# Kernel tuning notes

Measured on AMD Instinct MI355X. Metric: run time of the kernel, lower is better.

The kernel has to match this reference:

```python
import jax, jax.numpy as jnp
import numpy as np

N_DRUG, N_DIS = 100_000, 50_000
E1, E2 = 500_000, 250_000
D, H = 128, 4
HD = D // H          # 32
EAD, CONT, CARD = 32, 4, 8


def _segment_softmax(logits, seg, num_segments):
    # logits: [E, H], seg: [E] -> softmax normalized per destination node (PyG softmax)
    m = jax.ops.segment_max(logits, seg, num_segments=num_segments)
    m = jnp.where(jnp.isfinite(m), m, 0.0)  # empty segments
    ex = jnp.exp(logits - m[seg])
    s = jax.ops.segment_sum(ex, seg, num_segments=num_segments)
    return ex / (s[seg] + 1e-16)


def _edge_conv(src_x, dst_x, si, di, Wsrc, bsrc, Wdst, bdst, attn, gate):
    num_dst = dst_x.shape[0]
    msg_src = src_x[si] @ Wsrc + bsrc            # [E, D]
    msg_dst = dst_x[di] @ Wdst + bdst            # [E, D]
    msg = msg_src + msg_dst
    if gate is not None:
        msg = msg * gate
    E = msg.shape[0]
    mh = msg.reshape(E, H, HD)
    sh = msg_src.reshape(E, H, HD)
    dh = msg_dst.reshape(E, H, HD)
    logits = (sh * dh).sum(-1) * (1.0 / np.sqrt(HD)) + (mh * attn[None]).sum(-1)  # [E, H]
    w = _segment_softmax(logits, di, num_dst)    # [E, H]; dropout p applied only in training
    out = (mh * w[..., None]).reshape(E, D)
    return jax.ops.segment_sum(out, di, num_segments=num_dst)  # [num_dst, D]


def setup_inputs() -> dict:
    key = jax.random.key(0)
    it = iter(jax.random.split(key, 32))
    def nrm(shape, s=0.05):
        return jax.random.normal(next(it), shape, jnp.float32) * s
    def ri(hi, shape):
        return jax.random.randint(next(it), shape, 0, hi, jnp.int32)
    z = lambda n: jnp.zeros((n,), jnp.float32)
    return {
        "x_drug": nrm((N_DRUG, D), 1.0),
        "x_dis": nrm((N_DIS, D), 1.0),
        "e1_cont": nrm((E1, CONT), 1.0),
        "W_src1": nrm((D, D)), "b_src1": z(D),
        "W_dst1": nrm((D, D)), "b_dst1": z(D),
        "attn1": nrm((H, HD)),
        "emb1": nrm((CARD, EAD)),
        "gW1": nrm((EAD + CONT, D)), "gb1": z(D),
        "gW2": nrm((D, D)), "gb2": z(D),
        "W_src2": nrm((D, D)), "b_src2": z(D),
        "W_dst2": nrm((D, D)), "b_dst2": z(D),
        "attn2": nrm((H, HD)),
        "Wo_drug": nrm((D, D)), "bo_drug": z(D),
        "Wo_dis": nrm((D, D)), "bo_dis": z(D),
        "e1_src": ri(N_DRUG, (E1,)), "e1_dst": ri(N_DRUG, (E1,)),
        "e2_src": ri(N_DRUG, (E2,)), "e2_dst": ri(N_DIS, (E2,)),
        "e1_cat": ri(CARD, (E1,)),
    }


def reference(x_drug, x_dis, e1_cont, W_src1, b_src1, W_dst1, b_dst1, attn1,
              emb1, gW1, gb1, gW2, gb2, W_src2, b_src2, W_dst2, b_dst2, attn2,
              Wo_drug, bo_drug, Wo_dis, bo_dis,
              e1_src, e1_dst, e2_src, e2_dst, e1_cat):
    # drug -> drug edges, spec mixed (1 categorical + 4 continuous): gated messages
    gate_feat = jnp.concatenate([emb1[e1_cat], e1_cont], axis=-1)  # [E1, EAD+CONT]
    gate = jax.nn.sigmoid(
        jax.nn.gelu(gate_feat @ gW1 + gb1, approximate=False) @ gW2 + gb2)  # [E1, D]
    aggr_drug = _edge_conv(x_drug, x_drug, e1_src, e1_dst,
                           W_src1, b_src1, W_dst1, b_dst1, attn1, gate)
    # drug -> disease edges, spec none: no gate
    aggr_dis = _edge_conv(x_drug, x_dis, e2_src, e2_dst,
                          W_src2, b_src2, W_dst2, b_dst2, attn2, None)
    # one message list per dst node type -> mean over a single element == identity
    out_drug = aggr_drug @ Wo_drug + bo_drug
    out_dis = aggr_dis @ Wo_dis + bo_dis
    return (out_drug, out_dis)
```

## Files before the change

kernel.cpp:

```cpp
#include <hip/hip_runtime.h>
#include <hip/hip_bf16.h>
#include <math.h>

#define ND 100000
#define NS 50000
#define NE1 500000
#define NE2 250000
#define DIM 128
#define NH 4
#define HDI 32
#define GRID_M 512
#define GRID_G 1024
#define GRID_E1 2048
#define GRID_E2 1024
#define NT1 (NE1 / 16)
#define NT2 (NE2 / 16)

typedef __hip_bfloat16 bf16;
typedef unsigned short u16;
typedef unsigned int u32;
typedef short sx8 __attribute__((ext_vector_type(8)));
typedef float fx4 __attribute__((ext_vector_type(4)));

__device__ __forceinline__ float ldf(const float* p, size_t i) { return p[i]; }
__device__ __forceinline__ float ldf(const bf16* p, size_t i) { return __bfloat162float(p[i]); }
__device__ __forceinline__ float b2f(bf16 v) { return __bfloat162float(v); }

__device__ __forceinline__ u16 f2bfu(float f) {
    __hip_bfloat16 h = __float2bfloat16(f);
    union { __hip_bfloat16 b; u16 u; } c; c.b = h; return c.u;
}
__device__ __forceinline__ float2 bfp(u32 u) {
    float2 r;
    r.x = __uint_as_float(u << 16);
    r.y = __uint_as_float(u & 0xffff0000u);
    return r;
}
__device__ __forceinline__ sx8 pack8(float4 v0, float4 v1) {
    sx8 r;
    r[0] = (short)f2bfu(v0.x); r[1] = (short)f2bfu(v0.y);
    r[2] = (short)f2bfu(v0.z); r[3] = (short)f2bfu(v0.w);
    r[4] = (short)f2bfu(v1.x); r[5] = (short)f2bfu(v1.y);
    r[6] = (short)f2bfu(v1.z); r[7] = (short)f2bfu(v1.w);
    return r;
}
__device__ __forceinline__ sx8 lda8(const bf16* p) { return *(const sx8*)p; }
__device__ __forceinline__ sx8 lda8(const float* p) {
    return pack8(*(const float4*)p, *(const float4*)(p + 4));
}
__device__ __forceinline__ float4 ld4(const float* p) { return *(const float4*)p; }
__device__ __forceinline__ float4 ld4(const bf16* p) {
    float2 a = bfp(*(const u32*)p);
    float2 b = bfp(*(const u32*)(p + 2));
    return make_float4(a.x, a.y, b.x, b.y);
}

__device__ __forceinline__ float gelu_fast(float x) {
    float u2 = x * fmaf(x * x, 0.0713550f, 1.5957691f);
    u2 = fminf(u2, 40.0f);
    float t = __expf(u2);
    return x * t * __builtin_amdgcn_rcpf(t + 1.0f);
}
__device__ __forceinline__ float sigmoid_fast(float x) {
    return __builtin_amdgcn_rcpf(1.0f + __expf(-x));
}
__device__ __forceinline__ float exp_fast(float x) { return __expf(x); }

__device__ __forceinline__ void slab_store(float* Gw, const fx4* acc, int er, int lg) {
#pragma unroll
    for (int f = 0; f < 8; ++f)
#pragma unroll
        for (int r = 0; r < 4; ++r) {
            int row = 4 * lg + r;
            int byo = row * 512 + (((16 * f + er) * 4) ^ ((row & 7) << 4));
            *(float*)((char*)Gw + byo) = acc[f][r];
        }
}
__device__ __forceinline__ void slab_flush_bf16(const float* Gw, int lane, bf16* Yrow) {
#pragma unroll
    for (int i = 0; i < 16; ++i) {
        float2 gv = *(const float2*)((const char*)Gw + i * 512 + ((lane * 8) ^ ((i & 7) << 4)));
        u32 pk = ((u32)f2bfu(gv.y) << 16) | (u32)f2bfu(gv.x);
        *(u32*)&Yrow[(size_t)i * DIM + 2 * lane] = pk;
    }
}
__device__ __forceinline__ void sty2(float* p, float2 v) { *(float2*)p = v; }
__device__ __forceinline__ void sty2(bf16* p, float2 v) {
    *(u32*)p = ((u32)f2bfu(v.y) << 16) | (u32)f2bfu(v.x);
}

__global__ void fill16_kernel(u16* p, u16 v, size_t n) {
    size_t i = (size_t)blockIdx.x * blockDim.x + threadIdx.x;
    if (i < n) p[i] = v;
}

__global__ __launch_bounds__(64) void detect_kernel(const u16* w, int* flag) {
    int lane = threadIdx.x;
    int mx = 0;
    for (int j = 0; j < 32; ++j) {
        int i = 2 * (lane + 64 * j);
        int e = (w[i] >> 7) & 0xFF;
        mx = mx > e ? mx : e;
    }
    for (int d = 32; d; d >>= 1) { int o = __shfl_xor(mx, d); mx = mx > o ? mx : o; }
    if (lane == 0) flag[0] = (mx >= 0x90) ? 1 : 0;
}

__global__ __launch_bounds__(256) void hist_kernel(const int* __restrict__ dst, int ne,
                                                   u32* __restrict__ cnt) {
    int stride = gridDim.x * blockDim.x;
    for (int i = blockIdx.x * blockDim.x + threadIdx.x; i < ne; i += stride)
        atomicAdd(&cnt[dst[i]], 1u);
}

__global__ __launch_bounds__(256) void scanA_kernel(const u32* __restrict__ cnt, int nb,
                                                    u32* __restrict__ chk) {
    __shared__ u32 ws[4];
    int b = blockIdx.x, t = threadIdx.x;
    int i0 = b * 1024 + t * 4;
    u32 s = 0;
#pragma unroll
    for (int j = 0; j < 4; ++j) { int i = i0 + j; if (i < nb) s += cnt[i]; }
#pragma unroll
    for (int d = 1; d < 64; d <<= 1) s += __shfl_xor(s, d);
    if ((t & 63) == 0) ws[t >> 6] = s;
    __syncthreads();
    if (t == 0) chk[b] = ws[0] + ws[1] + ws[2] + ws[3];
}

__global__ __launch_bounds__(256) void scanB_kernel(u32* __restrict__ chk, int nc) {
    __shared__ u32 sh[256];
    int t = threadIdx.x;
    u32 v = (t < nc) ? chk[t] : 0u;
    sh[t] = v;
    __syncthreads();
    for (int d = 1; d < 256; d <<= 1) {
        u32 x = (t >= d) ? sh[t - d] : 0u;
        __syncthreads();
        if (t >= d) sh[t] += x;
        __syncthreads();
    }
    if (t < nc) chk[t] = sh[t] - v;
}

__global__ __launch_bounds__(256) void scanC_kernel(const u32* __restrict__ cnt, int nb,
                                                    const u32* __restrict__ chk,
                                                    u32* __restrict__ offs) {
    __shared__ u32 wsum[4];
    int b = blockIdx.x, t = threadIdx.x, lane = t & 63, wv = t >> 6;
    int i0 = b * 1024 + t * 4;
    u32 c0 = (i0 + 0 < nb) ? cnt[i0 + 0] : 0u;
    u32 c1 = (i0 + 1 < nb) ? cnt[i0 + 1] : 0u;
    u32 c2 = (i0 + 2 < nb) ? cnt[i0 + 2] : 0u;
    u32 c3 = (i0 + 3 < nb) ? cnt[i0 + 3] : 0u;
    u32 tot = c0 + c1 + c2 + c3;
    u32 inc = tot;
#pragma unroll
    for (int d = 1; d < 64; d <<= 1) { u32 x = __shfl_up(inc, d); if (lane >= d) inc += x; }
    if (lane == 63) wsum[wv] = inc;
    __syncthreads();
    u32 base = chk[b] + (inc - tot);
    for (int k = 0; k < wv; ++k) base += wsum[k];
    if (i0 + 0 < nb) offs[i0 + 0] = base;
    if (i0 + 1 < nb) offs[i0 + 1] = base + c0;
    if (i0 + 2 < nb) offs[i0 + 2] = base + c0 + c1;
    if (i0 + 3 < nb) offs[i0 + 3] = base + c0 + c1 + c2;
}

__global__ __launch_bounds__(256) void scatter_kernel(const int* __restrict__ dst, int ne,
                                                      u32* __restrict__ offs,
                                                      u32* __restrict__ perm) {
    int stride = gridDim.x * blockDim.x;
    for (int i = blockIdx.x * blockDim.x + threadIdx.x; i < ne; i += stride) {
        u32 p = atomicAdd(&offs[dst[i]], 1u);
        perm[p] = (u32)i;
    }
}

template <typename T>
__device__ __forceinline__ void transp(const T* W, u16* Bt, int gtid, int gstride) {
    for (int i = gtid; i < DIM * DIM; i += gstride) {
        int n = i >> 7, k = i & 127;
        Bt[i] = f2bfu(ldf(W, (size_t)k * DIM + n));
    }
}

template <typename T>
__device__ __forceinline__ void prep_body(
    const T* emb, const T* gW1, const T* gb1, const T* gW2,
    const T* Ws1, const T* Wd1, const T* Ws2, const T* Wd2, const T* Wod, const T* Wos,
    u16* B1t, float* gb2f, const T* gb2,
    u16* Btg, u16* Bs1, u16* Bd1, u16* Bs2, u16* Bd2, u16* Bod, u16* Bos)
{
    int gtid = blockIdx.x * blockDim.x + threadIdx.x;
    int gstride = gridDim.x * blockDim.x;
    for (int i = gtid; i < DIM * 32; i += gstride) {
        int n = i >> 5, k = i & 31;
        float v = 0.0f;
        if (k < 8) {
            v = ldf(gb1, n);
            for (int q = 0; q < 32; ++q) v += ldf(emb, k * 32 + q) * ldf(gW1, (size_t)q * DIM + n);
        } else if (k < 12) {
            v = ldf(gW1, (size_t)(32 + (k - 8)) * DIM + n);
        }
        B1t[i] = f2bfu(v);
    }
    for (int i = gtid; i < DIM; i += gstride) gb2f[i] = ldf(gb2, i);
    transp(gW2, Btg, gtid, gstride);
    transp(Ws1, Bs1, gtid, gstride);
    transp(Wd1, Bd1, gtid, gstride);
    transp(Ws2, Bs2, gtid, gstride);
    transp(Wd2, Bd2, gtid, gstride);
    transp(Wod, Bod, gtid, gstride);
    transp(Wos, Bos, gtid, gstride);
}

__global__ __launch_bounds__(256) void prep_kernel(
    const int* __restrict__ flag,
    const void* emb, const void* gW1, const void* gb1, const void* gW2, const void* gb2,
    const void* Ws1, const void* Wd1, const void* Ws2, const void* Wd2,
    const void* Wod, const void* Wos,
    u16* __restrict__ B1t, float* __restrict__ gb2f,
    u16* __restrict__ Btg, u16* __restrict__ Bs1, u16* __restrict__ Bd1,
    u16* __restrict__ Bs2, u16* __restrict__ Bd2, u16* __restrict__ Bod,
    u16* __restrict__ Bos)
{
    if (flag[0])
        prep_body((const float*)emb, (const float*)gW1, (const float*)gb1, (const float*)gW2,
                  (const float*)Ws1, (const float*)Wd1, (const float*)Ws2, (const float*)Wd2,
                  (const float*)Wod, (const float*)Wos,
                  B1t, gb2f, (const float*)gb2, Btg, Bs1, Bd1, Bs2, Bd2, Bod, Bos);
    else
        prep_body((const bf16*)emb, (const bf16*)gW1, (const bf16*)gb1, (const bf16*)gW2,
                  (const bf16*)Ws1, (const bf16*)Wd1, (const bf16*)Ws2, (const bf16*)Wd2,
                  (const bf16*)Wod, (const bf16*)Wos,
                  B1t, gb2f, (const bf16*)gb2, Btg, Bs1, Bd1, Bs2, Bd2, Bod, Bos);
}

template <typename T>
__device__ __forceinline__ void proj2m_body(
    float* Gw, const T* X, const T* b1, const T* b2,
    const u16* Bt1, const u16* Bt2, bf16* Y1, bf16* Y2, int N)
{
    int tid = threadIdx.x, lane = tid & 63, er = lane & 15, lg = lane >> 4;
    float c1i[8], c2i[8];
#pragma unroll
    for (int f = 0; f < 8; ++f) {
        c1i[f] = ldf(b1, 16 * f + er);
        c2i[f] = ldf(b2, 16 * f + er);
    }
    const int NW = GRID_M * 4;
    int gwid = blockIdx.x * 4 + (tid >> 6);
    int tiles = N / 16;
    for (int t = gwid; t < tiles; t += NW) {
        const T* xr = X + (size_t)(t * 16 + er) * DIM;
        sx8 a[4];
#pragma unroll
        for (int ks = 0; ks < 4; ++ks) a[ks] = lda8(xr + ks * 32 + lg * 8);
        fx4 acc1[8], acc2[8];
#pragma unroll
        for (int f = 0; f < 8; ++f) {
            acc1[f][0] = c1i[f]; acc1[f][1] = c1i[f]; acc1[f][2] = c1i[f]; acc1[f][3] = c1i[f];
            acc2[f][0] = c2i[f]; acc2[f][1] = c2i[f]; acc2[f][2] = c2i[f]; acc2[f][3] = c2i[f];
        }
#pragma unroll
        for (int ks = 0; ks < 4; ++ks)
#pragma unroll
            for (int f = 0; f < 8; ++f) {
                sx8 bv1 = *(const sx8*)(Bt1 + (size_t)(16 * f + er) * DIM + ks * 32 + lg * 8);
                acc1[f] = __builtin_amdgcn_mfma_f32_16x16x32_bf16(a[ks], bv1, acc1[f], 0, 0, 0);
                sx8 bv2 = *(const sx8*)(Bt2 + (size_t)(16 * f + er) * DIM + ks * 32 + lg * 8);
                acc2[f] = __builtin_amdgcn_mfma_f32_16x16x32_bf16(a[ks], bv2, acc2[f], 0, 0, 0);
            }
        slab_store(Gw, acc1, er, lg);
        slab_flush_bf16(Gw, lane, Y1 + (size_t)t * 16 * DIM);
        slab_store(Gw, acc2, er, lg);
        slab_flush_bf16(Gw, lane, Y2 + (size_t)t * 16 * DIM);
    }
}

__global__ __launch_bounds__(256) void proj2m_kernel(
    const int* __restrict__ flag, const void* X, const void* b1, const void* b2,
    const u16* __restrict__ Bt1, const u16* __restrict__ Bt2,
    bf16* __restrict__ Y1, bf16* __restrict__ Y2, int N)
{
    __shared__ float Gt[4][16 * 128];
    float* Gw = Gt[threadIdx.x >> 6];
    if (flag[0]) proj2m_body(Gw, (const float*)X, (const float*)b1, (const float*)b2, Bt1, Bt2, Y1, Y2, N);
    else         proj2m_body(Gw, (const bf16*)X, (const bf16*)b1, (const bf16*)b2, Bt1, Bt2, Y1, Y2, N);
}

template <typename T>
__device__ __forceinline__ void proj1m_body(
    float* Gw, const T* X, const T* b, const u16* Bt, bf16* Y, int N)
{
    int tid = threadIdx.x, lane = tid & 63, er = lane & 15, lg = lane >> 4;
    float ci[8];
#pragma unroll
    for (int f = 0; f < 8; ++f) ci[f] = ldf(b, 16 * f + er);
    const int NW = GRID_M * 4;
    int gwid = blockIdx.x * 4 + (tid >> 6);
    int tiles = N / 16;
    for (int t = gwid; t < tiles; t += NW) {
        const T* xr = X + (size_t)(t * 16 + er) * DIM;
        sx8 a[4];
#pragma unroll
        for (int ks = 0; ks < 4; ++ks) a[ks] = lda8(xr + ks * 32 + lg * 8);
        fx4 acc[8];
#pragma unroll
        for (int f = 0; f < 8; ++f) {
            acc[f][0] = ci[f]; acc[f][1] = ci[f]; acc[f][2] = ci[f]; acc[f][3] = ci[f];
        }
#pragma unroll
        for (int ks = 0; ks < 4; ++ks)
#pragma unroll
            for (int f = 0; f < 8; ++f) {
                sx8 bv = *(const sx8*)(Bt + (size_t)(16 * f + er) * DIM + ks * 32 + lg * 8);
                acc[f] = __builtin_amdgcn_mfma_f32_16x16x32_bf16(a[ks], bv, acc[f], 0, 0, 0);
            }
        slab_store(Gw, acc, er, lg);
        slab_flush_bf16(Gw, lane, Y + (size_t)t * 16 * DIM);
    }
}

__global__ __launch_bounds__(256) void proj1m_kernel(
    const int* __restrict__ flag, const void* X, const void* b,
    const u16* __restrict__ Bt, bf16* __restrict__ Y, int N)
{
    __shared__ float Gt[4][16 * 128];
    float* Gw = Gt[threadIdx.x >> 6];
    if (flag[0]) proj1m_body(Gw, (const float*)X, (const float*)b, Bt, Y, N);
    else         proj1m_body(Gw, (const bf16*)X, (const bf16*)b, Bt, Y, N);
}

template <typename T>
__device__ __forceinline__ void projoutm_body(
    float* Gw, const float* A, const float* s, const T* b,
    const u16* Bt, T* out, int N)
{
    int tid = threadIdx.x, lane = tid & 63, er = lane & 15, lg = lane >> 4;
    float ci[8];
#pragma unroll
    for (int f = 0; f < 8; ++f) ci[f] = ldf(b, 16 * f + er);
    const int NW = GRID_M * 4;
    int gwid = blockIdx.x * 4 + (tid >> 6);
    int tiles = N / 16;
    for (int t = gwid; t < tiles; t += NW) {
        const float* ar = A + (size_t)(t * 16 + er) * DIM;
        const float* sr = s + (size_t)(t * 16 + er) * NH;
        sx8 a[4];
#pragma unroll
        for (int ks = 0; ks < 4; ++ks) {
            float inv = 1.0f / (sr[ks] + 1e-16f);
            float4 v0 = *(const float4*)(ar + ks * 32 + lg * 8);
            float4 v1 = *(const float4*)(ar + ks * 32 + lg * 8 + 4);
            v0.x *= inv; v0.y *= inv; v0.z *= inv; v0.w *= inv;
            v1.x *= inv; v1.y *= inv; v1.z *= inv; v1.w *= inv;
            a[ks] = pack8(v0, v1);
        }
        fx4 acc[8];
#pragma unroll
        for (int f = 0; f < 8; ++f) {
            acc[f][0] = ci[f]; acc[f][1] = ci[f]; acc[f][2] = ci[f]; acc[f][3] = ci[f];
        }
#pragma unroll
        for (int ks = 0; ks < 4; ++ks)
#pragma unroll
            for (int f = 0; f < 8; ++f) {
                sx8 bv = *(const sx8*)(Bt + (size_t)(16 * f + er) * DIM + ks * 32 + lg * 8);
                acc[f] = __builtin_amdgcn_mfma_f32_16x16x32_bf16(a[ks], bv, acc[f], 0, 0, 0);
            }
        slab_store(Gw, acc, er, lg);
#pragma unroll
        for (int i = 0; i < 16; ++i) {
            float2 gv = *(const float2*)((const char*)Gw + i * 512 + ((lane * 8) ^ ((i & 7) << 4)));
            sty2(out + (size_t)(t * 16 + i) * DIM + 2 * lane, gv);
        }
    }
}

__global__ __launch_bounds__(256) void projoutm_kernel(
    const int* __restrict__ flag, const float* __restrict__ A, const float* __restrict__ s,
    const void* b, const u16* __restrict__ Bt, void* out, size_t off, int N)
{
    __shared__ float Gt[4][16 * 128];
    float* Gw = Gt[threadIdx.x >> 6];
    if (flag[0]) projoutm_body(Gw, A, s, (const float*)b, Bt, (float*)out + off, N);
    else         projoutm_body(Gw, A, s, (const bf16*)b, Bt, (bf16*)out + off, N);
}

template <typename T>
__device__ __forceinline__ void gateall_body(
    float* Gw, const int* cat, const T* econt,
    const float* gb2f, const u16* B1t, const u16* Btg,
    const u32* perm, u32* gates, int c0, int c1)
{
    int tid = threadIdx.x;
    int lane = tid & 63;
    int er = lane & 15, lg = lane >> 4;

    float cinit[8];
#pragma unroll
    for (int f = 0; f < 8; ++f) cinit[f] = gb2f[16 * f + er];

    const int NW = GRID_G * 4;
    int span = c1 - c0;
    int w = blockIdx.x * 4 + (tid >> 6);
    int tpw = (span + NW - 1) / NW;
    int t0 = c0 + w * tpw, t1 = t0 + tpw;
    if (t1 > c1) t1 = c1;

    const fx4 zf = {0.f, 0.f, 0.f, 0.f};

    for (int t = t0; t < t1; ++t) {
        int e = (int)perm[t * 16 + er];

        sx8 a1;
#pragma unroll
        for (int j = 0; j < 8; ++j) a1[j] = 0;
        if (lg == 0) {
            int c = cat[e];
#pragma unroll
            for (int j = 0; j < 8; ++j) a1[j] = (c == j) ? (short)0x3F80 : (short)0;
        } else if (lg == 1) {
            float4 fv = ld4(econt + (size_t)e * 4);
            a1[0] = (short)f2bfu(fv.x); a1[1] = (short)f2bfu(fv.y);
            a1[2] = (short)f2bfu(fv.z); a1[3] = (short)f2bfu(fv.w);
        }

        fx4 p1[8];
#pragma unroll
        for (int f = 0; f < 8; ++f) {
            sx8 b1 = *(const sx8*)(B1t + (size_t)(16 * f + er) * 32 + lg * 8);
            p1[f] = __builtin_amdgcn_mfma_f32_16x16x32_bf16(a1, b1, zf, 0, 0, 0);
        }

#pragma unroll
        for (int f = 0; f < 8; ++f)
#pragma unroll
            for (int r = 0; r < 4; ++r) {
                int row = 4 * lg + r;
                float hg = gelu_fast(p1[f][r]);
                int byo = row * 512 + (((16 * f + er) * 4) ^ ((row & 7) << 4));
                *(float*)((char*)Gw + byo) = hg;
            }

        sx8 a2[4];
#pragma unroll
        for (int ks = 0; ks < 4; ++ks) {
            int base = ks * 128 + lg * 32;
            float4 v0 = *(const float4*)((const char*)Gw + er * 512 + ((base)      ^ ((er & 7) << 4)));
            float4 v1 = *(const float4*)((const char*)Gw + er * 512 + ((base + 16) ^ ((er & 7) << 4)));
            a2[ks] = pack8(v0, v1);
        }

        fx4 acc[8];
#pragma unroll
        for (int f = 0; f < 8; ++f) {
            acc[f][0] = cinit[f]; acc[f][1] = cinit[f];
            acc[f][2] = cinit[f]; acc[f][3] = cinit[f];
        }
#pragma unroll
        for (int ks = 0; ks < 4; ++ks) {
#pragma unroll
            for (int f = 0; f < 8; ++f) {
                sx8 b = *(const sx8*)(Btg + (size_t)(16 * f + er) * DIM + ks * 32 + lg * 8);
                acc[f] = __builtin_amdgcn_mfma_f32_16x16x32_bf16(a2[ks], b, acc[f], 0, 0, 0);
            }
        }

#pragma unroll
        for (int f = 0; f < 8; ++f)
#pragma unroll
            for (int r = 0; r < 4; ++r) {
                int row = 4 * lg + r;
                float g = sigmoid_fast(acc[f][r]);
                int byo = row * 512 + (((16 * f + er) * 4) ^ ((row & 7) << 4));
                *(float*)((char*)Gw + byo) = g;
            }

#pragma unroll
        for (int i = 0; i < 16; ++i) {
            float2 gv = *(const float2*)((const char*)Gw + i * 512 + ((lane * 8) ^ ((i & 7) << 4)));
            u32 pk = ((u32)f2bfu(gv.y) << 16) | (u32)f2bfu(gv.x);
            gates[((size_t)(t - c0) * 16 + i) * 64 + lane] = pk;
        }
    }
}

__global__ __launch_bounds__(256) void gateall_kernel(
    const int* __restrict__ flag, const int* __restrict__ cat, const void* econt,
    const float* __restrict__ gb2f, const u16* __restrict__ B1t,
    const u16* __restrict__ Btg,
    const u32* __restrict__ perm, u32* __restrict__ gates, int c0, int c1)
{
    __shared__ float Gt[4][16 * 128];
    float* Gw = Gt[threadIdx.x >> 6];
    if (flag[0]) gateall_body(Gw, cat, (const float*)econt, gb2f, B1t, Btg, perm, gates, c0, c1);
    else         gateall_body(Gw, cat, (const bf16*)econt, gb2f, B1t, Btg, perm, gates, c0, c1);
}

template <typename T>
__device__ __forceinline__ void edge1e_body(
    const bf16* Xs, const bf16* Xd,
    const int* src, const int* dst,
    const T* attn, const u32* perm, const u32* gates, int c0, int c1,
    float* s_out, float* aggr)
{
    int tid = threadIdx.x;
    int lane = tid & 63;
    int d0 = 2 * lane, h = lane >> 4, k0 = d0 & 31;
    float av0 = ldf(attn, h * HDI + k0), av1 = ldf(attn, h * HDI + k0 + 1);
    const float rs = 0.17677669529663688110f;

    const int NW = GRID_E1 * 4;
    int span = c1 - c0;
    int w = blockIdx.x * 4 + (tid >> 6);
    int cpw = (span + NW - 1) / NW;
    int t0 = c0 + w * cpw, t1 = t0 + cpw;
    if (t1 > c1) t1 = c1;

    int cur_di = -1;
    float acc0 = 0.f, acc1 = 0.f, ssum = 0.f;

    for (int t = t0; t < t1; ++t) {
        u32 pe = 0, sv = 0, dv = 0;
        if (lane < 16) {
            pe = perm[t * 16 + lane];
            sv = (u32)src[(int)pe];
            dv = (u32)dst[(int)pe];
        }
        u32 xsp[16], xdp[16], gp[16];
#pragma unroll
        for (int i = 0; i < 16; ++i) {
            int si = (int)__builtin_amdgcn_readlane(sv, i);
            int di = (int)__builtin_amdgcn_readlane(dv, i);
            xsp[i] = *(const u32*)&Xs[(size_t)si * DIM + d0];
            xdp[i] = *(const u32*)&Xd[(size_t)di * DIM + d0];
            gp[i]  = gates[((size_t)(t - c0) * 16 + i) * 64 + lane];
        }
#pragma unroll
        for (int i = 0; i < 16; ++i) {
            int di = (int)__builtin_amdgcn_readlane(dv, i);
            float2 sxy = bfp(xsp[i]);
            float2 dxy = bfp(xdp[i]);
            float2 gxy = bfp(gp[i]);
            if (di != cur_di) {
                if (cur_di >= 0) {
                    float* ap = &aggr[(size_t)cur_di * DIM + d0];
                    atomicAdd(ap, acc0);
                    atomicAdd(ap + 1, acc1);
                    if ((lane & 15) == 0)
                        atomicAdd(&s_out[(size_t)cur_di * NH + h], ssum);
                }
                cur_di = di; acc0 = 0.f; acc1 = 0.f; ssum = 0.f;
            }
            float m0 = (sxy.x + dxy.x) * gxy.x;
            float m1 = (sxy.y + dxy.y) * gxy.y;
            float p = (sxy.x * dxy.x + sxy.y * dxy.y) * rs + m0 * av0 + m1 * av1;
            p += __shfl_xor(p, 8);
            p += __shfl_xor(p, 4);
            p += __shfl_xor(p, 2);
            p += __shfl_xor(p, 1);
            float ev = exp_fast(fminf(p, 80.0f));
            acc0 = fmaf(ev, m0, acc0);
            acc1 = fmaf(ev, m1, acc1);
            ssum += ev;
        }
    }
    if (cur_di >= 0) {
        float* ap = &aggr[(size_t)cur_di * DIM + d0];
        atomicAdd(ap, acc0);
        atomicAdd(ap + 1, acc1);
        if ((lane & 15) == 0)
            atomicAdd(&s_out[(size_t)cur_di * NH + h], ssum);
    }
}

__global__ __launch_bounds__(256) void edge1e_kernel(
    const int* __restrict__ flag,
    const bf16* __restrict__ Xs, const bf16* __restrict__ Xd,
    const int* __restrict__ src, const int* __restrict__ dst,
    const void* attn, const u32* __restrict__ perm, const u32* __restrict__ gates,
    int c0, int c1, float* __restrict__ s_out, float* __restrict__ aggr)
{
    if (flag[0]) edge1e_body(Xs, Xd, src, dst, (const float*)attn, perm, gates, c0, c1, s_out, aggr);
    else         edge1e_body(Xs, Xd, src, dst, (const bf16*)attn, perm, gates, c0, c1, s_out, aggr);
}

template <typename T>
__device__ __forceinline__ void edge2e_body(
    const bf16* Xs, const bf16* Xd,
    const int* src, const int* dst,
    const T* attn, const u32* perm, float* s_out, float* aggr)
{
    int tid = threadIdx.x;
    int lane = tid & 63;
    int d0 = 2 * lane, h = lane >> 4, k0 = d0 & 31;
    float av0 = ldf(attn, h * HDI + k0), av1 = ldf(attn, h * HDI + k0 + 1);
    const float rs = 0.17677669529663688110f;

    const int NW = GRID_E2 * 4;
    int w = blockIdx.x * 4 + (tid >> 6);
    int cpw = (NT2 + NW - 1) / NW;
    int t0 = w * cpw, t1 = t0 + cpw;
    if (t1 > NT2) t1 = NT2;

    int cur_di = -1;
    float acc0 = 0.f, acc1 = 0.f, ssum = 0.f;

    for (int t = t0; t < t1; ++t) {
        u32 pe = 0, sv = 0, dv = 0;
        if (lane < 16) {
            pe = perm[t * 16 + lane];
            sv = (u32)src[(int)pe];
            dv = (u32)dst[(int)pe];
        }
        u32 xsp[16], xdp[16];
#pragma unroll
        for (int i = 0; i < 16; ++i) {
            int si = (int)__builtin_amdgcn_readlane(sv, i);
            int di = (int)__builtin_amdgcn_readlane(dv, i);
            xsp[i] = *(const u32*)&Xs[(size_t)si * DIM + d0];
            xdp[i] = *(const u32*)&Xd[(size_t)di * DIM + d0];
        }
#pragma unroll
        for (int i = 0; i < 16; ++i) {
            int di = (int)__builtin_amdgcn_readlane(dv, i);
            float2 sxy = bfp(xsp[i]);
            float2 dxy = bfp(xdp[i]);
            if (di != cur_di) {
                if (cur_di >= 0) {
                    float* ap = &aggr[(size_t)cur_di * DIM + d0];
                    atomicAdd(ap, acc0);
                    atomicAdd(ap + 1, acc1);
                    if ((lane & 15) == 0)
                        atomicAdd(&s_out[(size_t)cur_di * NH + h], ssum);
                }
                cur_di = di; acc0 = 0.f; acc1 = 0.f; ssum = 0.f;
            }
            float m0 = sxy.x + dxy.x;
            float m1 = sxy.y + dxy.y;
            float p = (sxy.x * dxy.x + sxy.y * dxy.y) * rs + m0 * av0 + m1 * av1;
            p += __shfl_xor(p, 8);
            p += __shfl_xor(p, 4);
            p += __shfl_xor(p, 2);
            p += __shfl_xor(p, 1);
            float ev = exp_fast(fminf(p, 80.0f));
            acc0 = fmaf(ev, m0, acc0);
            acc1 = fmaf(ev, m1, acc1);
            ssum += ev;
        }
    }
    if (cur_di >= 0) {
        float* ap = &aggr[(size_t)cur_di * DIM + d0];
        atomicAdd(ap, acc0);
        atomicAdd(ap + 1, acc1);
        if ((lane & 15) == 0)
            atomicAdd(&s_out[(size_t)cur_di * NH + h], ssum);
    }
}

__global__ __launch_bounds__(256) void edge2e_kernel(
    const int* __restrict__ flag,
    const bf16* __restrict__ Xs, const bf16* __restrict__ Xd,
    const int* __restrict__ src, const int* __restrict__ dst,
    const void* attn, const u32* __restrict__ perm,
    float* __restrict__ s_out, float* __restrict__ aggr)
{
    if (flag[0]) edge2e_body(Xs, Xd, src, dst, (const float*)attn, perm, s_out, aggr);
    else         edge2e_body(Xs, Xd, src, dst, (const bf16*)attn, perm, s_out, aggr);
}

extern "C" void kernel_launch(void* const* d_in, const int* in_sizes, int n_in,
                              void* d_out, int out_size, void* d_ws, size_t ws_size,
                              hipStream_t stream)
{
    const void* x_drug  = d_in[0];
    const void* x_dis   = d_in[1];
    const void* e1_cont = d_in[2];
    const void* W_src1  = d_in[3];
    const void* b_src1  = d_in[4];
    const void* W_dst1  = d_in[5];
    const void* b_dst1  = d_in[6];
    const void* attn1   = d_in[7];
    const void* emb1    = d_in[8];
    const void* gW1     = d_in[9];
    const void* gb1     = d_in[10];
    const void* gW2     = d_in[11];
    const void* gb2     = d_in[12];
    const void* W_src2  = d_in[13];
    const void* b_src2  = d_in[14];
    const void* W_dst2  = d_in[15];
    const void* b_dst2  = d_in[16];
    const void* attn2   = d_in[17];
    const void* Wo_drug = d_in[18];
    const void* bo_drug = d_in[19];
    const void* Wo_dis  = d_in[20];
    const void* bo_dis  = d_in[21];
    const int* e1_src = (const int*)d_in[22];
    const int* e1_dst = (const int*)d_in[23];
    const int* e2_src = (const int*)d_in[24];
    const int* e2_dst = (const int*)d_in[25];
    const int* e1_cat = (const int*)d_in[26];

    bool sizes_ok = (n_in == 27)
        && in_sizes[0] == ND * DIM && in_sizes[1] == NS * DIM
        && in_sizes[2] == NE1 * 4
        && in_sizes[3] == DIM * DIM && in_sizes[4] == DIM
        && in_sizes[5] == DIM * DIM && in_sizes[6] == DIM
        && in_sizes[7] == NH * HDI && in_sizes[8] == 8 * 32
        && in_sizes[9] == 36 * DIM && in_sizes[10] == DIM
        && in_sizes[11] == DIM * DIM && in_sizes[12] == DIM
        && in_sizes[13] == DIM * DIM && in_sizes[17] == NH * HDI
        && in_sizes[18] == DIM * DIM && in_sizes[20] == DIM * DIM
        && in_sizes[22] == NE1 && in_sizes[23] == NE1
        && in_sizes[24] == NE2 && in_sizes[25] == NE2 && in_sizes[26] == NE1;
    if (!sizes_ok) {
        size_t n = (size_t)out_size;
        fill16_kernel<<<(int)((n + 255) / 256), 256, 0, stream>>>((u16*)d_out, 0x429A, n);
        return;
    }

    size_t off_B1   = 64;
    size_t off_g2   = off_B1 + (size_t)DIM * 32 * 2;
    size_t off_Bt   = off_g2 + DIM * 4;
    size_t off_Bs1  = off_Bt  + (size_t)DIM * DIM * 2;
    size_t off_Bd1  = off_Bs1 + (size_t)DIM * DIM * 2;
    size_t off_Bs2  = off_Bd1 + (size_t)DIM * DIM * 2;
    size_t off_Bd2  = off_Bs2 + (size_t)DIM * DIM * 2;
    size_t off_Bod  = off_Bd2 + (size_t)DIM * DIM * 2;
    size_t off_Bos  = off_Bod + (size_t)DIM * DIM * 2;
    size_t off_Xs   = off_Bos + (size_t)DIM * DIM * 2;
    size_t off_Xd   = off_Xs + (size_t)ND * DIM * 2;
    size_t off_sb   = off_Xd + (size_t)ND * DIM * 2;
    size_t off_aggr = off_sb + (size_t)ND * NH * 4;
    size_t off_cnt  = off_aggr + (size_t)ND * DIM * 4;
    size_t off_offs = off_cnt + (size_t)(ND + 16) * 4;
    size_t off_chk  = off_offs + (size_t)(ND + 16) * 4;
    size_t off_p1   = off_chk + 512;
    size_t off_p2   = off_p1 + (size_t)NE1 * 4;
    size_t off_gate = (off_p2 + (size_t)NE2 * 4 + 255) & ~(size_t)255;
    if (ws_size < off_gate) {
        size_t n = (size_t)out_size;
        fill16_kernel<<<(int)((n + 255) / 256), 256, 0, stream>>>((u16*)d_out, 0x42F6, n);
        return;
    }

    int nparts = 0, cpp = 0;
    for (int p = 1; p <= 32; p <<= 1) {
        int c = (NT1 + p - 1) / p;
        if (off_gate + (size_t)c * 16 * 256 <= ws_size) { nparts = p; cpp = c; break; }
    }
    if (!nparts) {
        size_t n = (size_t)out_size;
        fill16_kernel<<<(int)((n + 255) / 256), 256, 0, stream>>>((u16*)d_out, 0x42F6, n);
        return;
    }

    char* w = (char*)d_ws;
    int*   flag = (int*)w;
    u16*   B1t  = (u16*)(w + off_B1);
    float* gb2p = (float*)(w + off_g2);
    u16*   Btg  = (u16*)(w + off_Bt);
    u16*   Bs1  = (u16*)(w + off_Bs1);
    u16*   Bd1  = (u16*)(w + off_Bd1);
    u16*   Bs2  = (u16*)(w + off_Bs2);
    u16*   Bd2  = (u16*)(w + off_Bd2);
    u16*   Bod  = (u16*)(w + off_Bod);
    u16*   Bos  = (u16*)(w + off_Bos);
    bf16*  Xs   = (bf16*)(w + off_Xs);
    bf16*  Xd   = (bf16*)(w + off_Xd);
    float* sb   = (float*)(w + off_sb);
    float* aggr = (float*)(w + off_aggr);
    u32*   cnt  = (u32*)(w + off_cnt);
    u32*   offs = (u32*)(w + off_offs);
    u32*   chk  = (u32*)(w + off_chk);
    u32*   perm1 = (u32*)(w + off_p1);
    u32*   perm2 = (u32*)(w + off_p2);
    u32*   gates = (u32*)(w + off_gate);

    detect_kernel<<<1, 64, 0, stream>>>((const u16*)W_src1, flag);
    prep_kernel<<<64, 256, 0, stream>>>(flag, emb1, gW1, gb1, gW2, gb2,
                                        W_src1, W_dst1, W_src2, W_dst2, Wo_drug, Wo_dis,
                                        B1t, gb2p, Btg, Bs1, Bd1, Bs2, Bd2, Bod, Bos);

    hipMemsetAsync(cnt, 0, (size_t)(ND + 16) * 4, stream);
    hist_kernel<<<1024, 256, 0, stream>>>(e1_dst, NE1, cnt);
    scanA_kernel<<<98, 256, 0, stream>>>(cnt, ND, chk);
    scanB_kernel<<<1, 256, 0, stream>>>(chk, 98);
    scanC_kernel<<<98, 256, 0, stream>>>(cnt, ND, chk, offs);
    scatter_kernel<<<1024, 256, 0, stream>>>(e1_dst, NE1, offs, perm1);

    hipMemsetAsync(sb, 0, (size_t)ND * NH * 4, stream);
    hipMemsetAsync(aggr, 0, (size_t)ND * DIM * 4, stream);
    proj2m_kernel<<<GRID_M, 256, 0, stream>>>(flag, x_drug, b_src1, b_dst1, Bs1, Bd1, Xs, Xd, ND);
    for (int part = 0; part < nparts; ++part) {
        int c0 = part * cpp, c1 = c0 + cpp;
        if (c1 > NT1) c1 = NT1;
        if (c0 >= c1) break;
        gateall_kernel<<<GRID_G, 256, 0, stream>>>(flag, e1_cat, e1_cont,
                                                   gb2p, B1t, Btg, perm1, gates, c0, c1);
        edge1e_kernel<<<GRID_E1, 256, 0, stream>>>(flag, Xs, Xd, e1_src, e1_dst,
                                                   attn1, perm1, gates, c0, c1, sb, aggr);
    }
    projoutm_kernel<<<GRID_M, 256, 0, stream>>>(flag, aggr, sb, bo_drug, Bod, d_out, 0, ND);

    hipMemsetAsync(cnt, 0, (size_t)(NS + 16) * 4, stream);
    hist_kernel<<<1024, 256, 0, stream>>>(e2_dst, NE2, cnt);
    scanA_kernel<<<49, 256, 0, stream>>>(cnt, NS, chk);
    scanB_kernel<<<1, 256, 0, stream>>>(chk, 49);
    scanC_kernel<<<49, 256, 0, stream>>>(cnt, NS, chk, offs);
    scatter_kernel<<<1024, 256, 0, stream>>>(e2_dst, NE2, offs, perm2);

    hipMemsetAsync(sb, 0, (size_t)NS * NH * 4, stream);
    hipMemsetAsync(aggr, 0, (size_t)NS * DIM * 4, stream);
    proj1m_kernel<<<GRID_M, 256, 0, stream>>>(flag, x_drug, b_src2, Bs2, Xs, ND);
    proj1m_kernel<<<GRID_M, 256, 0, stream>>>(flag, x_dis, b_dst2, Bd2, Xd, NS);
    edge2e_kernel<<<GRID_E2, 256, 0, stream>>>(flag, Xs, Xd, e2_src, e2_dst, attn2, perm2, sb, aggr);
    projoutm_kernel<<<GRID_M, 256, 0, stream>>>(flag, aggr, sb, bo_dis, Bos, d_out, (size_t)ND * DIM, NS);
}
```

Measured before the change: 716.7 us.

## Fuse gate MLP computation into drug-edge attention kernel, dropping gate buffer

The gate MLP (two MFMA GEMMs plus GELU/sigmoid) now runs inside the edge-1 aggregation kernel, and the sigmoid outputs are read straight from shared memory instead of a global bf16 gates buffer. This removes the write and re-read of a 500K x 128 bf16 gate tensor, the partitioned launch loop and its workspace requirement. In exchange, the edge kernel carries more registers and shared memory (16 KB per block), which may lower occupancy for the latency-bound gather and atomic work. Gates also stay in fp32 rather than being rounded to bf16.

```diff
diff --git a/kernel.cpp b/kernel.cpp
--- a/kernel.cpp
+++ b/kernel.cpp
@@ -10,7 +10,6 @@
 #define NH 4
 #define HDI 32
 #define GRID_M 512
-#define GRID_G 1024
 #define GRID_E1 2048
 #define GRID_E2 1024
 #define NT1 (NE1 / 16)
@@ -390,31 +389,50 @@
 }
 
 template <typename T>
-__device__ __forceinline__ void gateall_body(
-    float* Gw, const int* cat, const T* econt,
-    const float* gb2f, const u16* B1t, const u16* Btg,
-    const u32* perm, u32* gates, int c0, int c1)
+__device__ __forceinline__ void edge1f_body(
+    float* Gw, const bf16* Xs, const bf16* Xd,
+    const int* src, const int* dst, const int* cat, const T* econt,
+    const T* attn, const float* gb2f, const u16* B1t, const u16* Btg,
+    const u32* perm, float* s_out, float* aggr)
 {
     int tid = threadIdx.x;
     int lane = tid & 63;
     int er = lane & 15, lg = lane >> 4;
+    int d0 = 2 * lane, h = lane >> 4, k0 = d0 & 31;
+    float av0 = ldf(attn, h * HDI + k0), av1 = ldf(attn, h * HDI + k0 + 1);
+    const float rs = 0.17677669529663688110f;
 
     float cinit[8];
 #pragma unroll
     for (int f = 0; f < 8; ++f) cinit[f] = gb2f[16 * f + er];
 
-    const int NW = GRID_G * 4;
-    int span = c1 - c0;
+    const int NW = GRID_E1 * 4;
     int w = blockIdx.x * 4 + (tid >> 6);
-    int tpw = (span + NW - 1) / NW;
-    int t0 = c0 + w * tpw, t1 = t0 + tpw;
-    if (t1 > c1) t1 = c1;
-
+    int cpw = (NT1 + NW - 1) / NW;
+    int t0 = w * cpw, t1 = t0 + cpw;
+    if (t1 > NT1) t1 = NT1;
+
+    int cur_di = -1;
+    float acc0 = 0.f, acc1 = 0.f, ssum = 0.f;
     const fx4 zf = {0.f, 0.f, 0.f, 0.f};
 
     for (int t = t0; t < t1; ++t) {
-        int e = (int)perm[t * 16 + er];
-
+        u32 pe = 0, sv = 0, dv = 0;
+        if (lane < 16) {
+            pe = perm[t * 16 + lane];
+            sv = (u32)src[(int)pe];
+            dv = (u32)dst[(int)pe];
+        }
+        u32 xsp[16], xdp[16];
+#pragma unroll
+        for (int i = 0; i < 16; ++i) {
+            int si = (int)__builtin_amdgcn_readlane(sv, i);
+            int di = (int)__builtin_amdgcn_readlane(dv, i);
+            xsp[i] = *(const u32*)&Xs[(size_t)si * DIM + d0];
+            xdp[i] = *(const u32*)&Xd[(size_t)di * DIM + d0];
+        }
+
+        int e = __shfl((int)pe, er);
         sx8 a1;
 #pragma unroll
         for (int j = 0; j < 8; ++j) a1[j] = 0;
@@ -454,18 +472,18 @@
             a2[ks] = pack8(v0, v1);
         }
 
-        fx4 acc[8];
+        fx4 gacc[8];
 #pragma unroll
         for (int f = 0; f < 8; ++f) {
-            acc[f][0] = cinit[f]; acc[f][1] = cinit[f];
-            acc[f][2] = cinit[f]; acc[f][3] = cinit[f];
+            gacc[f][0] = cinit[f]; gacc[f][1] = cinit[f];
+            gacc[f][2] = cinit[f]; gacc[f][3] = cinit[f];
         }
 #pragma unroll
         for (int ks = 0; ks < 4; ++ks) {
 #pragma unroll
             for (int f = 0; f < 8; ++f) {
                 sx8 b = *(const sx8*)(Btg + (size_t)(16 * f + er) * DIM + ks * 32 + lg * 8);
-                acc[f] = __builtin_amdgcn_mfma_f32_16x16x32_bf16(a2[ks], b, acc[f], 0, 0, 0);
+                gacc[f] = __builtin_amdgcn_mfma_f32_16x16x32_bf16(a2[ks], b, gacc[f], 0, 0, 0);
             }
         }
 
@@ -474,77 +492,21 @@
 #pragma unroll
             for (int r = 0; r < 4; ++r) {
                 int row = 4 * lg + r;
-                float g = sigmoid_fast(acc[f][r]);
+                float g = sigmoid_fast(gacc[f][r]);
                 int byo = row * 512 + (((16 * f + er) * 4) ^ ((row & 7) << 4));
                 *(float*)((char*)Gw + byo) = g;
             }
 
-#pragma unroll
-        for (int i = 0; i < 16; ++i) {
-            float2 gv = *(const float2*)((const char*)Gw + i * 512 + ((lane * 8) ^ ((i & 7) << 4)));
-            u32 pk = ((u32)f2bfu(gv.y) << 16) | (u32)f2bfu(gv.x);
-            gates[((size_t)(t - c0) * 16 + i) * 64 + lane] = pk;
-        }
-    }
-}
-
-__global__ __launch_bounds__(256) void gateall_kernel(
-    const int* __restrict__ flag, const int* __restrict__ cat, const void* econt,
-    const float* __restrict__ gb2f, const u16* __restrict__ B1t,
-    const u16* __restrict__ Btg,
-    const u32* __restrict__ perm, u32* __restrict__ gates, int c0, int c1)
-{
-    __shared__ float Gt[4][16 * 128];
-    float* Gw = Gt[threadIdx.x >> 6];
-    if (flag[0]) gateall_body(Gw, cat, (const float*)econt, gb2f, B1t, Btg, perm, gates, c0, c1);
-    else         gateall_body(Gw, cat, (const bf16*)econt, gb2f, B1t, Btg, perm, gates, c0, c1);
-}
-
-template <typename T>
-__device__ __forceinline__ void edge1e_body(
-    const bf16* Xs, const bf16* Xd,
-    const int* src, const int* dst,
-    const T* attn, const u32* perm, const u32* gates, int c0, int c1,
-    float* s_out, float* aggr)
-{
-    int tid = threadIdx.x;
-    int lane = tid & 63;
-    int d0 = 2 * lane, h = lane >> 4, k0 = d0 & 31;
-    float av0 = ldf(attn, h * HDI + k0), av1 = ldf(attn, h * HDI + k0 + 1);
-    const float rs = 0.17677669529663688110f;
-
-    const int NW = GRID_E1 * 4;
-    int span = c1 - c0;
-    int w = blockIdx.x * 4 + (tid >> 6);
-    int cpw = (span + NW - 1) / NW;
-    int t0 = c0 + w * cpw, t1 = t0 + cpw;
-    if (t1 > c1) t1 = c1;
-
-    int cur_di = -1;
-    float acc0 = 0.f, acc1 = 0.f, ssum = 0.f;
-
-    for (int t = t0; t < t1; ++t) {
-        u32 pe = 0, sv = 0, dv = 0;
-        if (lane < 16) {
-            pe = perm[t * 16 + lane];
-            sv = (u32)src[(int)pe];
-            dv = (u32)dst[(int)pe];
-        }
-        u32 xsp[16], xdp[16], gp[16];
-#pragma unroll
-        for (int i = 0; i < 16; ++i) {
-            int si = (int)__builtin_amdgcn_readlane(sv, i);
-            int di = (int)__builtin_amdgcn_readlane(dv, i);
-            xsp[i] = *(const u32*)&Xs[(size_t)si * DIM + d0];
-            xdp[i] = *(const u32*)&Xd[(size_t)di * DIM + d0];
-            gp[i]  = gates[((size_t)(t - c0) * 16 + i) * 64 + lane];
-        }
+        float2 gvp[16];
+#pragma unroll
+        for (int i = 0; i < 16; ++i)
+            gvp[i] = *(const float2*)((const char*)Gw + i * 512 + ((lane * 8) ^ ((i & 7) << 4)));
+
 #pragma unroll
         for (int i = 0; i < 16; ++i) {
             int di = (int)__builtin_amdgcn_readlane(dv, i);
             float2 sxy = bfp(xsp[i]);
             float2 dxy = bfp(xdp[i]);
-            float2 gxy = bfp(gp[i]);
             if (di != cur_di) {
                 if (cur_di >= 0) {
                     float* ap = &aggr[(size_t)cur_di * DIM + d0];
@@ -555,8 +517,8 @@
                 }
                 cur_di = di; acc0 = 0.f; acc1 = 0.f; ssum = 0.f;
             }
-            float m0 = (sxy.x + dxy.x) * gxy.x;
-            float m1 = (sxy.y + dxy.y) * gxy.y;
+            float m0 = (sxy.x + dxy.x) * gvp[i].x;
+            float m1 = (sxy.y + dxy.y) * gvp[i].y;
             float p = (sxy.x * dxy.x + sxy.y * dxy.y) * rs + m0 * av0 + m1 * av1;
             p += __shfl_xor(p, 8);
             p += __shfl_xor(p, 4);
@@ -577,15 +539,23 @@
     }
 }
 
-__global__ __launch_bounds__(256) void edge1e_kernel(
+__global__ __launch_bounds__(256) void edge1f_kernel(
     const int* __restrict__ flag,
     const bf16* __restrict__ Xs, const bf16* __restrict__ Xd,
     const int* __restrict__ src, const int* __restrict__ dst,
-    const void* attn, const u32* __restrict__ perm, const u32* __restrict__ gates,
-    int c0, int c1, float* __restrict__ s_out, float* __restrict__ aggr)
-{
-    if (flag[0]) edge1e_body(Xs, Xd, src, dst, (const float*)attn, perm, gates, c0, c1, s_out, aggr);
-    else         edge1e_body(Xs, Xd, src, dst, (const bf16*)attn, perm, gates, c0, c1, s_out, aggr);
+    const int* __restrict__ cat, const void* econt, const void* attn,
+    const float* __restrict__ gb2f, const u16* __restrict__ B1t,
+    const u16* __restrict__ Btg, const u32* __restrict__ perm,
+    float* __restrict__ s_out, float* __restrict__ aggr)
+{
+    __shared__ float Gt[4][16 * 128];
+    float* Gw = Gt[threadIdx.x >> 6];
+    if (flag[0])
+        edge1f_body(Gw, Xs, Xd, src, dst, cat, (const float*)econt, (const float*)attn,
+                    gb2f, B1t, Btg, perm, s_out, aggr);
+    else
+        edge1f_body(Gw, Xs, Xd, src, dst, cat, (const bf16*)econt, (const bf16*)attn,
+                    gb2f, B1t, Btg, perm, s_out, aggr);
 }
 
 template <typename T>
@@ -740,19 +710,8 @@
     size_t off_chk  = off_offs + (size_t)(ND + 16) * 4;
     size_t off_p1   = off_chk + 512;
     size_t off_p2   = off_p1 + (size_t)NE1 * 4;
-    size_t off_gate = (off_p2 + (size_t)NE2 * 4 + 255) & ~(size_t)255;
-    if (ws_size < off_gate) {
-        size_t n = (size_t)out_size;
-        fill16_kernel<<<(int)((n + 255) / 256), 256, 0, stream>>>((u16*)d_out, 0x42F6, n);
-        return;
-    }
-
-    int nparts = 0, cpp = 0;
-    for (int p = 1; p <= 32; p <<= 1) {
-        int c = (NT1 + p - 1) / p;
-        if (off_gate + (size_t)c * 16 * 256 <= ws_size) { nparts = p; cpp = c; break; }
-    }
-    if (!nparts) {
+    size_t need     = off_p2 + (size_t)NE2 * 4;
+    if (ws_size < need) {
         size_t n = (size_t)out_size;
         fill16_kernel<<<(int)((n + 255) / 256), 256, 0, stream>>>((u16*)d_out, 0x42F6, n);
         return;
@@ -778,7 +737,6 @@
     u32*   chk  = (u32*)(w + off_chk);
     u32*   perm1 = (u32*)(w + off_p1);
     u32*   perm2 = (u32*)(w + off_p2);
-    u32*   gates = (u32*)(w + off_gate);
 
     detect_kernel<<<1, 64, 0, stream>>>((const u16*)W_src1, flag);
     prep_kernel<<<64, 256, 0, stream>>>(flag, emb1, gW1, gb1, gW2, gb2,
@@ -795,15 +753,8 @@
     hipMemsetAsync(sb, 0, (size_t)ND * NH * 4, stream);
     hipMemsetAsync(aggr, 0, (size_t)ND * DIM * 4, stream);
     proj2m_kernel<<<GRID_M, 256, 0, stream>>>(flag, x_drug, b_src1, b_dst1, Bs1, Bd1, Xs, Xd, ND);
-    for (int part = 0; part < nparts; ++part) {
-        int c0 = part * cpp, c1 = c0 + cpp;
-        if (c1 > NT1) c1 = NT1;
-        if (c0 >= c1) break;
-        gateall_kernel<<<GRID_G, 256, 0, stream>>>(flag, e1_cat, e1_cont,
-                                                   gb2p, B1t, Btg, perm1, gates, c0, c1);
-        edge1e_kernel<<<GRID_E1, 256, 0, stream>>>(flag, Xs, Xd, e1_src, e1_dst,
-                                                   attn1, perm1, gates, c0, c1, sb, aggr);
-    }
+    edge1f_kernel<<<GRID_E1, 256, 0, stream>>>(flag, Xs, Xd, e1_src, e1_dst, e1_cat,
+                                               e1_cont, attn1, gb2p, B1t, Btg, perm1, sb, aggr);
     projoutm_kernel<<<GRID_M, 256, 0, stream>>>(flag, aggr, sb, bo_drug, Bod, d_out, 0, ND);
 
     hipMemsetAsync(cnt, 0, (size_t)(NS + 16) * 4, stream);
```

Result: slower. 736.8 us (+2.8%).
